# Kernel optimization log

Hardware: AMD Instinct MI355X
Metric: run time of the kernel (lower is better)

Reference implementation:

```python
import jax, jax.numpy as jnp
import numpy as np

BLOCK = 16                      # NVFP4 block size along K
FP4_MAX = 6.0                   # e2m1 max magnitude
FP8_MAX = 448.0                 # e4m3 max
E2M1_GRID = jnp.array([0.0, 0.5, 1.0, 1.5, 2.0, 3.0, 4.0, 5.0, 6.0], dtype=jnp.float32)
E2M1_MIDS = jnp.array([0.25, 0.75, 1.25, 1.75, 2.5, 3.5, 4.5, 5.5], dtype=jnp.float32)


def _global_sf(t):
    # 448*6 / amax(|t|), amax clamped to 1e-12 (matches torch code)
    amax = jnp.clip(jnp.max(jnp.abs(jnp.nan_to_num(t))), 1e-12, None)
    return (FP8_MAX * FP4_MAX) / amax


def _round_e4m3(v):
    # round-to-nearest e4m3fn via dtype cast
    return v.astype(jnp.float8_e4m3fn).astype(jnp.float32)


def _round_e2m1(v):
    # nearest value on the signed e2m1 grid, clamped to +-6
    a = jnp.clip(jnp.abs(v), 0.0, FP4_MAX)
    idx = jnp.searchsorted(E2M1_MIDS, a)
    return E2M1_GRID[idx] * jnp.sign(v)


def nvfp4_quant_dequant(t, global_sf):
    """Simulate nvfp4_quantize + dequant. Returns t_hat ~= t * global_sf
    (values representable as e2m1 * e4m3 block scale)."""
    rows, K = t.shape
    tb = t.reshape(rows, K // BLOCK, BLOCK)
    amax = jnp.max(jnp.abs(tb), axis=-1, keepdims=True)            # [rows, K/16, 1]
    sf = _round_e4m3(jnp.clip(amax * global_sf / FP4_MAX, 0.0, FP8_MAX))
    inv_sf = jnp.where(sf > 0, global_sf / sf, 0.0)
    q = _round_e2m1(tb * inv_sf)                                   # fp4 codes (as f32)
    return (q * sf).reshape(rows, K)                               # dequant in scaled space


def setup_inputs() -> dict:
    key = jax.random.key(0)
    kx, kw = jax.random.split(key)
    M, K, N = 4096, 4096, 4096
    x = jax.random.normal(kx, (M, K), dtype=jnp.float32)
    w = jax.random.normal(kw, (N, K), dtype=jnp.float32)
    return {"x": x, "w": w}


def reference(x, w):
    w_gsf = _global_sf(w)
    x_gsf = _global_sf(x)
    w_hat = nvfp4_quant_dequant(w, w_gsf)   # ~= w * w_gsf
    x_hat = nvfp4_quant_dequant(x, x_gsf)   # ~= x * x_gsf
    alpha = 1.0 / (w_gsf * x_gsf)
    # mm_fp4: (x_q xsf) @ (w_q wsf)^T * alpha  -> [M, N]
    return jnp.einsum('mk,nk->mn', x_hat, w_hat) * alpha
```

## Files before the change

### kernel.cpp

```cpp
#include <hip/hip_runtime.h>
#include <hip/hip_bf16.h>
#include <stdint.h>

#define M_DIM 4096
#define N_DIM 4096
#define K_DIM 4096
#define KB 8192

typedef __bf16 bf16x8 __attribute__((ext_vector_type(8)));
typedef float  f32x4  __attribute__((ext_vector_type(4)));

__global__ __launch_bounds__(256) void amax2_kernel(const float* __restrict__ x,
                                                    const float* __restrict__ w,
                                                    unsigned int* __restrict__ out) {
    __shared__ float red[4];
    const int half = blockIdx.x >> 10;
    const float4* in4 = (const float4*)(half ? w : x);
    const int lid = (blockIdx.x & 1023) * 256 + threadIdx.x;
    const int S = 1024 * 256;
    float m0 = 0.f, m1 = 0.f, m2 = 0.f, m3 = 0.f;
#pragma unroll
    for (int k = 0; k < 4; ++k) {
        float4 a = in4[lid + (4 * k + 0) * S];
        float4 b = in4[lid + (4 * k + 1) * S];
        float4 c = in4[lid + (4 * k + 2) * S];
        float4 d = in4[lid + (4 * k + 3) * S];
        m0 = fmaxf(m0, fmaxf(fmaxf(fabsf(a.x), fabsf(a.y)), fmaxf(fabsf(a.z), fabsf(a.w))));
        m1 = fmaxf(m1, fmaxf(fmaxf(fabsf(b.x), fabsf(b.y)), fmaxf(fabsf(b.z), fabsf(b.w))));
        m2 = fmaxf(m2, fmaxf(fmaxf(fabsf(c.x), fabsf(c.y)), fmaxf(fabsf(c.z), fabsf(c.w))));
        m3 = fmaxf(m3, fmaxf(fmaxf(fabsf(d.x), fabsf(d.y)), fmaxf(fabsf(d.z), fabsf(d.w))));
    }
    float m = fmaxf(fmaxf(m0, m1), fmaxf(m2, m3));
#pragma unroll
    for (int off = 32; off > 0; off >>= 1)
        m = fmaxf(m, __shfl_xor(m, off, 64));
    if ((threadIdx.x & 63) == 0) red[threadIdx.x >> 6] = m;
    __syncthreads();
    if (threadIdx.x == 0) {
        float r = fmaxf(fmaxf(red[0], red[1]), fmaxf(red[2], red[3]));
        atomicMax(out + half, __float_as_uint(r));
    }
}

__device__ __forceinline__ float round_e4m3(float v) {
    if (!(v > 0.f)) return 0.f;
    uint32_t u = __float_as_uint(v);
    int e = (int)(u >> 23) - 127;
    if (e < -6) e = -6;
    float ulp     = __uint_as_float((uint32_t)(e - 3 + 127) << 23);
    float inv_ulp = __uint_as_float((uint32_t)(3 - e + 127) << 23);
    return rintf(v * inv_ulp) * ulp;
}

__device__ __forceinline__ float round_e2m1_mag(float a) {
    float q = 0.f;
    q = (a > 0.25f) ? 0.5f : q;
    q = (a > 0.75f) ? 1.0f : q;
    q = (a > 1.25f) ? 1.5f : q;
    q = (a > 1.75f) ? 2.0f : q;
    q = (a > 2.5f)  ? 3.0f : q;
    q = (a > 3.5f)  ? 4.0f : q;
    q = (a > 4.5f)  ? 5.0f : q;
    q = (a > 5.5f)  ? 6.0f : q;
    return q;
}

__device__ __forceinline__ unsigned int pack2(float va, float vb, float inv, float sf) {
    float xa = va * inv, xb = vb * inv;
    float qa = round_e2m1_mag(fminf(fabsf(xa), 6.f));
    float qb = round_e2m1_mag(fminf(fabsf(xb), 6.f));
    float ta = copysignf(qa, xa) * sf;
    float tb = copysignf(qb, xb) * sf;
    return (__float_as_uint(ta) >> 16) | ((__float_as_uint(tb) >> 16) << 16);
}

__global__ __launch_bounds__(256) void quant2_kernel(const float* __restrict__ x,
                                                     const float* __restrict__ w,
                                                     unsigned short* __restrict__ xq,
                                                     unsigned short* __restrict__ wq,
                                                     const unsigned int* __restrict__ amax_bits) {
    const float gx = 2688.0f / fmaxf(__uint_as_float(amax_bits[0]), 1e-12f);
    const float gw = 2688.0f / fmaxf(__uint_as_float(amax_bits[1]), 1e-12f);
    const int t0 = blockIdx.x * 256 + threadIdx.x;
    const int S = 4096 * 256;
#pragma unroll
    for (int it = 0; it < 8; ++it) {
        const bool isx = (it < 4);
        const float4* src = (const float4*)(isx ? x : w);
        unsigned short* dst = isx ? xq : wq;
        const float gsf = isx ? gx : gw;
        const int li = t0 + (isx ? it : it - 4) * S;
        float4 v = src[li];
        float am = fmaxf(fmaxf(fabsf(v.x), fabsf(v.y)), fmaxf(fabsf(v.z), fabsf(v.w)));
        am = fmaxf(am, __shfl_xor(am, 1, 64));
        am = fmaxf(am, __shfl_xor(am, 2, 64));
        float sf  = round_e4m3(fminf(fmaxf(am * gsf / 6.0f, 0.f), 448.0f));
        float inv = (sf > 0.f) ? (gsf / sf) : 0.f;
        uint2 o;
        o.x = pack2(v.x, v.y, inv, sf);
        o.y = pack2(v.z, v.w, inv, sf);
        *(uint2*)(dst + (size_t)li * 4) = o;
    }
}


__global__ __launch_bounds__(512, 2) void gemm_kernel(const unsigned short* __restrict__ A,
                                                      const unsigned short* __restrict__ B,
                                                      float* __restrict__ C,
                                                      const unsigned int* __restrict__ amax_bits) {
    __shared__ alignas(16) char smem[131072];

    const int tid  = threadIdx.x;
    const int lane = tid & 63;
    const int wid  = tid >> 6;
    const int wr   = wid >> 2;
    const int wc   = wid & 3;

    int bid = blockIdx.x;
    int swz = (bid & 7) * 32 + (bid >> 3);
    const int brow = (swz >> 4) * 256;
    const int bcol = (swz & 15) * 256;

    int rowS[2], colS[2], Lr[2];
#pragma unroll
    for (int r = 0; r < 2; ++r) {
        int L = r * 8192 + tid * 16;
        int b = L ^ (((L >> 7) & 7) << 4);
        Lr[r] = L;
        rowS[r] = b >> 7;
        colS[r] = b & 127;
    }
    const char* Abase = (const char*)A;
    const char* Bbase = (const char*)B;

    auto STAGE = [&](int ts, int slot) {
        const char* mat = (slot >= 2) ? Abase : Bbase;
        int rbase = ((slot >= 2) ? brow : bcol) + ((slot & 1) ? 128 : 0);
        int loff  = (ts & 1) * 65536 + ((slot >= 2) ? 0 : 32768) + ((slot & 1) ? 16384 : 0);
#pragma unroll
        for (int r = 0; r < 2; ++r) {
            const char* gp = mat + (size_t)(rbase + rowS[r]) * KB + ts * 128 + colS[r];
            __builtin_amdgcn_global_load_lds(
                (const __attribute__((address_space(1))) unsigned int*)gp,
                (__attribute__((address_space(3))) unsigned int*)(smem + loff + Lr[r]),
                16, 0, 0);
        }
    };

    const int lr  = lane & 15;
    const int kg  = lane >> 4;
    const int swx = (lr & 7) << 4;
    int colA[2];
#pragma unroll
    for (int ks = 0; ks < 2; ++ks) colA[ks] = (ks * 64 + kg * 16) ^ swx;
    int rowAb[8], rowBb[4];
#pragma unroll
    for (int m = 0; m < 8; ++m) rowAb[m] = (wr * 128 + m * 16 + lr) * 128;
#pragma unroll
    for (int n = 0; n < 4; ++n) rowBb[n] = 32768 + (wc * 64 + n * 16 + lr) * 128;

    bf16x8 aR[4][2];
    bf16x8 bR[4][2];
    f32x4  acc[8][4];
#pragma unroll
    for (int m = 0; m < 8; ++m)
#pragma unroll
        for (int n = 0; n < 4; ++n)
#pragma unroll
            for (int j = 0; j < 4; ++j) acc[m][n][j] = 0.f;

    auto LDA = [&](int bufo, int mg) {
#pragma unroll
        for (int mm = 0; mm < 4; ++mm)
#pragma unroll
            for (int ks = 0; ks < 2; ++ks)
                aR[mm][ks] = *(const bf16x8*)(smem + bufo + rowAb[mg * 4 + mm] + colA[ks]);
    };
    auto LDB = [&](int bufo, int ng) {
#pragma unroll
        for (int nn = 0; nn < 2; ++nn)
#pragma unroll
            for (int ks = 0; ks < 2; ++ks)
                bR[ng * 2 + nn][ks] = *(const bf16x8*)(smem + bufo + rowBb[ng * 2 + nn] + colA[ks]);
    };
    auto MMA = [&](int mg, int ng) {
        __builtin_amdgcn_s_setprio(1);
#pragma unroll
        for (int ks = 0; ks < 2; ++ks)
#pragma unroll
            for (int mm = 0; mm < 4; ++mm)
#pragma unroll
                for (int nn = 0; nn < 2; ++nn) {
                    int m = mg * 4 + mm, n = ng * 2 + nn;
                    acc[m][n] = __builtin_amdgcn_mfma_f32_16x16x32_bf16(aR[mm][ks], bR[n][ks], acc[m][n], 0, 0, 0);
                }
        __builtin_amdgcn_s_setprio(0);
    };

    STAGE(0, 0); STAGE(0, 1); STAGE(0, 2); STAGE(0, 3);
    asm volatile("s_waitcnt vmcnt(4)" ::: "memory");
    STAGE(1, 0); STAGE(1, 1); STAGE(1, 2);
    asm volatile("s_waitcnt vmcnt(6)" ::: "memory");
    __builtin_amdgcn_s_barrier();

#pragma unroll 1
    for (int i = 0; i < 32; ++i) {
        int t0 = 2 * i;
        int n2 = (t0 + 2 < 64) ? t0 + 2 : 63;
        int n3 = (t0 + 3 < 64) ? t0 + 3 : 63;

        LDA(0, 0); LDB(0, 0); STAGE(t0 + 1, 3);
        __builtin_amdgcn_s_barrier();
        asm volatile("s_waitcnt lgkmcnt(0)" ::: "memory");
        MMA(0, 0);
        __builtin_amdgcn_s_barrier();

        LDB(0, 1); STAGE(n2, 0);
        __builtin_amdgcn_s_barrier();
        asm volatile("s_waitcnt lgkmcnt(0)" ::: "memory");
        MMA(0, 1);
        __builtin_amdgcn_s_barrier();

        LDA(0, 1); STAGE(n2, 1);
        __builtin_amdgcn_s_barrier();
        asm volatile("s_waitcnt lgkmcnt(0)" ::: "memory");
        MMA(1, 1);
        __builtin_amdgcn_s_barrier();

        STAGE(n2, 2);
        asm volatile("s_waitcnt vmcnt(6)" ::: "memory");
        __builtin_amdgcn_s_barrier();
        MMA(1, 0);
        __builtin_amdgcn_s_barrier();

        LDA(65536, 0); LDB(65536, 0); STAGE(n2, 3);
        __builtin_amdgcn_s_barrier();
        asm volatile("s_waitcnt lgkmcnt(0)" ::: "memory");
        MMA(0, 0);
        __builtin_amdgcn_s_barrier();

        LDB(65536, 1); STAGE(n3, 0);
        __builtin_amdgcn_s_barrier();
        asm volatile("s_waitcnt lgkmcnt(0)" ::: "memory");
        MMA(0, 1);
        __builtin_amdgcn_s_barrier();

        LDA(65536, 1); STAGE(n3, 1);
        __builtin_amdgcn_s_barrier();
        asm volatile("s_waitcnt lgkmcnt(0)" ::: "memory");
        MMA(1, 1);
        __builtin_amdgcn_s_barrier();

        STAGE(n3, 2);
        asm volatile("s_waitcnt vmcnt(6)" ::: "memory");
        __builtin_amdgcn_s_barrier();
        MMA(1, 0);
        __builtin_amdgcn_s_barrier();
    }

    float ax = fmaxf(__uint_as_float(amax_bits[0]), 1e-12f);
    float aw = fmaxf(__uint_as_float(amax_bits[1]), 1e-12f);
    float alpha = 1.0f / ((2688.0f / ax) * (2688.0f / aw));
    const int r4 = kg * 4;
    const int cn = lane & 15;
#pragma unroll
    for (int m = 0; m < 8; ++m)
#pragma unroll
        for (int n = 0; n < 4; ++n)
#pragma unroll
            for (int j = 0; j < 4; ++j) {
                int row = brow + wr * 128 + m * 16 + r4 + j;
                int col = bcol + wc * 64 + n * 16 + cn;
                C[(size_t)row * N_DIM + col] = acc[m][n][j] * alpha;
            }
}

extern "C" void kernel_launch(void* const* d_in, const int* in_sizes, int n_in,
                              void* d_out, int out_size, void* d_ws, size_t ws_size,
                              hipStream_t stream) {
    const float* x = (const float*)d_in[0];
    const float* w = (const float*)d_in[1];
    float* out = (float*)d_out;

    unsigned int*   amax  = (unsigned int*)d_ws;
    unsigned short* x_hat = (unsigned short*)((char*)d_ws + 256);
    unsigned short* w_hat = x_hat + (size_t)M_DIM * K_DIM;

    hipMemsetAsync(d_ws, 0, 256, stream);

    hipLaunchKernelGGL(amax2_kernel, dim3(2048), dim3(256), 0, stream, x, w, amax);
    hipLaunchKernelGGL(quant2_kernel, dim3(4096), dim3(256), 0, stream, x, w, x_hat, w_hat,
                       (const unsigned int*)amax);
    hipLaunchKernelGGL(gemm_kernel, dim3(256), dim3(512), 0, stream,
                       x_hat, w_hat, out, (const unsigned int*)d_ws);
}
```

Baseline: 181.0 us.

## Software-pipeline LDS A-fragment loads with MFMA using register double buffering

Reorganizes the GEMM main loop so that each phase loads the next 32-row A chunk into one of two register buffers while MFMAs run on the other. All B fragments for a K-tile are loaded at once. The per-phase lgkmcnt(0) waits and the extra barrier around each MMA block are removed. This is meant to hide LDS latency behind matrix work and cut synchronisation, at the cost of more live registers and a more fragile ordering between the async global-to-LDS stages and LDS reads.

```diff
diff --git a/kernel.cpp b/kernel.cpp
--- a/kernel.cpp
+++ b/kernel.cpp
@@ -103,7 +103,6 @@
     }
 }
 
-
 __global__ __launch_bounds__(512, 2) void gemm_kernel(const unsigned short* __restrict__ A,
                                                       const unsigned short* __restrict__ B,
                                                       float* __restrict__ C,
@@ -159,8 +158,8 @@
 #pragma unroll
     for (int n = 0; n < 4; ++n) rowBb[n] = 32768 + (wc * 64 + n * 16 + lr) * 128;
 
-    bf16x8 aR[4][2];
     bf16x8 bR[4][2];
+    bf16x8 aS0[2][2], aS1[2][2];
     f32x4  acc[8][4];
 #pragma unroll
     for (int m = 0; m < 8; ++m)
@@ -169,31 +168,30 @@
 #pragma unroll
             for (int j = 0; j < 4; ++j) acc[m][n][j] = 0.f;
 
-    auto LDA = [&](int bufo, int mg) {
-#pragma unroll
-        for (int mm = 0; mm < 4; ++mm)
+    auto LDB_ALL = [&](int bufo) {
+#pragma unroll
+        for (int n = 0; n < 4; ++n)
 #pragma unroll
             for (int ks = 0; ks < 2; ++ks)
-                aR[mm][ks] = *(const bf16x8*)(smem + bufo + rowAb[mg * 4 + mm] + colA[ks]);
-    };
-    auto LDB = [&](int bufo, int ng) {
-#pragma unroll
-        for (int nn = 0; nn < 2; ++nn)
+                bR[n][ks] = *(const bf16x8*)(smem + bufo + rowBb[n] + colA[ks]);
+    };
+    auto LDC = [&](int bufo, int ci, bf16x8 (&s)[2][2]) {
+#pragma unroll
+        for (int mm = 0; mm < 2; ++mm)
 #pragma unroll
             for (int ks = 0; ks < 2; ++ks)
-                bR[ng * 2 + nn][ks] = *(const bf16x8*)(smem + bufo + rowBb[ng * 2 + nn] + colA[ks]);
-    };
-    auto MMA = [&](int mg, int ng) {
+                s[mm][ks] = *(const bf16x8*)(smem + bufo + rowAb[ci * 2 + mm] + colA[ks]);
+    };
+    auto MMAc = [&](int ci, bf16x8 (&s)[2][2]) {
         __builtin_amdgcn_s_setprio(1);
 #pragma unroll
         for (int ks = 0; ks < 2; ++ks)
 #pragma unroll
-            for (int mm = 0; mm < 4; ++mm)
-#pragma unroll
-                for (int nn = 0; nn < 2; ++nn) {
-                    int m = mg * 4 + mm, n = ng * 2 + nn;
-                    acc[m][n] = __builtin_amdgcn_mfma_f32_16x16x32_bf16(aR[mm][ks], bR[n][ks], acc[m][n], 0, 0, 0);
-                }
+            for (int mm = 0; mm < 2; ++mm)
+#pragma unroll
+                for (int n = 0; n < 4; ++n)
+                    acc[ci * 2 + mm][n] =
+                        __builtin_amdgcn_mfma_f32_16x16x32_bf16(s[mm][ks], bR[n][ks], acc[ci * 2 + mm][n], 0, 0, 0);
         __builtin_amdgcn_s_setprio(0);
     };
 
@@ -202,59 +200,32 @@
     STAGE(1, 0); STAGE(1, 1); STAGE(1, 2);
     asm volatile("s_waitcnt vmcnt(6)" ::: "memory");
     __builtin_amdgcn_s_barrier();
+    LDC(0, 0, aS0); LDB_ALL(0); STAGE(1, 3);
+    __builtin_amdgcn_s_barrier();
 
 #pragma unroll 1
     for (int i = 0; i < 32; ++i) {
-        int t0 = 2 * i;
-        int n2 = (t0 + 2 < 64) ? t0 + 2 : 63;
-        int n3 = (t0 + 3 < 64) ? t0 + 3 : 63;
-
-        LDA(0, 0); LDB(0, 0); STAGE(t0 + 1, 3);
-        __builtin_amdgcn_s_barrier();
-        asm volatile("s_waitcnt lgkmcnt(0)" ::: "memory");
-        MMA(0, 0);
-        __builtin_amdgcn_s_barrier();
-
-        LDB(0, 1); STAGE(n2, 0);
-        __builtin_amdgcn_s_barrier();
-        asm volatile("s_waitcnt lgkmcnt(0)" ::: "memory");
-        MMA(0, 1);
-        __builtin_amdgcn_s_barrier();
-
-        LDA(0, 1); STAGE(n2, 1);
-        __builtin_amdgcn_s_barrier();
-        asm volatile("s_waitcnt lgkmcnt(0)" ::: "memory");
-        MMA(1, 1);
-        __builtin_amdgcn_s_barrier();
-
-        STAGE(n2, 2);
+        int e = 2 * i;
+        int n2 = (e + 2 < 64) ? e + 2 : 63;
+        int n3 = (e + 3 < 64) ? e + 3 : 63;
+
+        LDC(0, 1, aS1); MMAc(0, aS0); STAGE(n2, 0);
+        __builtin_amdgcn_s_barrier();
+        LDC(0, 2, aS0); MMAc(1, aS1); STAGE(n2, 1);
+        __builtin_amdgcn_s_barrier();
+        LDC(0, 3, aS1); MMAc(2, aS0); STAGE(n2, 2);
         asm volatile("s_waitcnt vmcnt(6)" ::: "memory");
         __builtin_amdgcn_s_barrier();
-        MMA(1, 0);
-        __builtin_amdgcn_s_barrier();
-
-        LDA(65536, 0); LDB(65536, 0); STAGE(n2, 3);
-        __builtin_amdgcn_s_barrier();
-        asm volatile("s_waitcnt lgkmcnt(0)" ::: "memory");
-        MMA(0, 0);
-        __builtin_amdgcn_s_barrier();
-
-        LDB(65536, 1); STAGE(n3, 0);
-        __builtin_amdgcn_s_barrier();
-        asm volatile("s_waitcnt lgkmcnt(0)" ::: "memory");
-        MMA(0, 1);
-        __builtin_amdgcn_s_barrier();
-
-        LDA(65536, 1); STAGE(n3, 1);
-        __builtin_amdgcn_s_barrier();
-        asm volatile("s_waitcnt lgkmcnt(0)" ::: "memory");
-        MMA(1, 1);
-        __builtin_amdgcn_s_barrier();
-
-        STAGE(n3, 2);
+        LDC(65536, 0, aS0); MMAc(3, aS1); LDB_ALL(65536); STAGE(n2, 3);
+        __builtin_amdgcn_s_barrier();
+        LDC(65536, 1, aS1); MMAc(0, aS0); STAGE(n3, 0);
+        __builtin_amdgcn_s_barrier();
+        LDC(65536, 2, aS0); MMAc(1, aS1); STAGE(n3, 1);
+        __builtin_amdgcn_s_barrier();
+        LDC(65536, 3, aS1); MMAc(2, aS0); STAGE(n3, 2);
         asm volatile("s_waitcnt vmcnt(6)" ::: "memory");
         __builtin_amdgcn_s_barrier();
-        MMA(1, 0);
+        LDC(0, 0, aS0); MMAc(3, aS1); LDB_ALL(0); STAGE(n3, 3);
         __builtin_amdgcn_s_barrier();
     }
 
```

Result: faster. 174.0 us (-3.9%).
